# Optimization experiments

Hardware: AMD Instinct MI355X
Metric: run time of the kernel (lower is better)

Reference implementation:

```python
import jax, jax.numpy as jnp
import numpy as np

EMBED = 1024
HEADS = 16
HEAD_DIM = EMBED // HEADS
NEG = -1e20


def setup_inputs() -> dict:
    key = jax.random.key(0)
    ks = jax.random.split(key, 12)
    N, S, E = 2, 2048, EMBED
    w = lambda k: (jax.random.normal(k, (E, E), dtype=jnp.float32) * 0.02)
    b = lambda k: (jax.random.normal(k, (E,), dtype=jnp.float32) * 0.02)
    return {
        "values": jax.random.normal(ks[0], (N, S, E), dtype=jnp.float32),
        "keys": jax.random.normal(ks[1], (N, S, E), dtype=jnp.float32),
        "query": jax.random.normal(ks[2], (N, S, E), dtype=jnp.float32),
        "mask": jnp.ones((N, S), dtype=jnp.int32),
        "Wv": w(ks[3]), "bv": b(ks[4]),
        "Wk": w(ks[5]), "bk": b(ks[6]),
        "Wq": w(ks[7]), "bq": b(ks[8]),
        "Wo": w(ks[9]), "bo": b(ks[10]),
    }


def reference(values, keys, query, mask, Wv, bv, Wk, bk, Wq, bq, Wo, bo):
    N, S, E = query.shape
    # torch nn.Linear: x @ W.T + b
    v = (values @ Wv.T + bv).reshape(N, S, HEADS, HEAD_DIM)
    k = (keys @ Wk.T + bk).reshape(N, S, HEADS, HEAD_DIM)
    q = (query @ Wq.T + bq).reshape(N, S, HEADS, HEAD_DIM)
    # full [N,H,Q,K] score matrix, as in the original einsum
    energy = jnp.einsum('nqhd,nkhd->nhqk', q, k)
    # 2D mask with mismatched dims triggers causal tril path in the original
    causal = jnp.tril(jnp.ones((S, S), dtype=bool))  # [Q,K]
    energy = jnp.where(causal[None, None, :, :], energy, NEG)
    # NOTE: original scales by sqrt(embed_size), not sqrt(head_dim)
    attn = jax.nn.softmax(energy / jnp.sqrt(jnp.float32(E)), axis=3)
    out = jnp.einsum('nhqk,nkhd->nqhd', attn, v).reshape(N, S, E)
    return out @ Wo.T + bo
```

## Files before the change

kernel.cpp:

```cpp
#include <hip/hip_runtime.h>

typedef __bf16 bf16;
typedef __bf16 bf16x4 __attribute__((ext_vector_type(4)));
typedef __bf16 bf16x8 __attribute__((ext_vector_type(8)));
typedef float floatx4 __attribute__((ext_vector_type(4)));

#define GLOAD_LDS16(gp, lp) \
  __builtin_amdgcn_global_load_lds( \
      (const __attribute__((address_space(1))) void*)(gp), \
      (__attribute__((address_space(3))) void*)(lp), 16, 0, 0)

__global__ __launch_bounds__(256) void cvt_all_kernel(
    const float* __restrict__ v, const float* __restrict__ k, const float* __restrict__ q,
    const float* __restrict__ wv, const float* __restrict__ wk,
    const float* __restrict__ wq, const float* __restrict__ wo,
    bf16* __restrict__ xv, bf16* __restrict__ xk, bf16* __restrict__ xq,
    bf16* __restrict__ bwv, bf16* __restrict__ bwk, bf16* __restrict__ bwq,
    bf16* __restrict__ bwo) {
  const int i = blockIdx.x * 256 + threadIdx.x;
  const int A4 = 1 << 20;
  const float* src; bf16* dst; int off;
  if (i < A4)            { src = v; dst = xv; off = i; }
  else if (i < 2 * A4)   { src = k; dst = xk; off = i - A4; }
  else if (i < 3 * A4)   { src = q; dst = xq; off = i - 2 * A4; }
  else {
    int j = i - 3 * A4; int r = j >> 18; off = j & ((1 << 18) - 1);
    src = (r == 0) ? wv : (r == 1) ? wk : (r == 2) ? wq : wo;
    dst = (r == 0) ? bwv : (r == 1) ? bwk : (r == 2) ? bwq : bwo;
  }
  float4 x = reinterpret_cast<const float4*>(src)[off];
  union { bf16 b[4]; short4 s; } u;
  u.b[0] = (bf16)x.x; u.b[1] = (bf16)x.y; u.b[2] = (bf16)x.z; u.b[3] = (bf16)x.w;
  reinterpret_cast<short4*>(dst)[off] = u.s;
}

template <int MODE>
__device__ __forceinline__ void gemm_body(
    const bf16* __restrict__ A, const bf16* __restrict__ B,
    const float* __restrict__ bias, void* __restrict__ Cout,
    int bx, int by) {
  constexpr int K = 1024, N = 1024;
  __shared__ __align__(16) bf16 SMEM[8192];
  bf16* As = SMEM;
  bf16* Bs = SMEM + 4096;
  const int tid = threadIdx.x;
  const int lane = tid & 63;
  const int wave = tid >> 6;
  const int quad = lane >> 4;
  const int l16 = lane & 15;
  const int wm = (wave >> 1) * 64;
  const int wn = (wave & 1) * 64;
  const int am0 = by * 128;
  const int bn0 = bx * 128;
  const int srow = lane >> 2;
  const int scol = (lane & 3) * 8;

  floatx4 acc[4][4] = {};

  for (int k0 = 0; k0 < K; k0 += 32) {
    __syncthreads();
#pragma unroll
    for (int j = 0; j < 2; j++) {
      const int chunk = wave * 2 + j;
      const int row = chunk * 16 + srow;
      GLOAD_LDS16(A + (size_t)(am0 + row) * K + k0 + scol, As + chunk * 512);
      GLOAD_LDS16(B + (size_t)(bn0 + row) * K + k0 + scol, Bs + chunk * 512);
    }
    __syncthreads();

    bf16x8 af[4], bfv[4];
#pragma unroll
    for (int mi = 0; mi < 4; mi++)
      af[mi] = *reinterpret_cast<const bf16x8*>(&As[(wm + mi * 16 + l16) * 32 + quad * 8]);
#pragma unroll
    for (int ni = 0; ni < 4; ni++)
      bfv[ni] = *reinterpret_cast<const bf16x8*>(&Bs[(wn + ni * 16 + l16) * 32 + quad * 8]);
#pragma unroll
    for (int mi = 0; mi < 4; mi++)
#pragma unroll
      for (int ni = 0; ni < 4; ni++)
        acc[mi][ni] = __builtin_amdgcn_mfma_f32_16x16x32_bf16(af[mi], bfv[ni], acc[mi][ni], 0, 0, 0);
  }

  if constexpr (MODE == 2) {
#pragma unroll
    for (int mi = 0; mi < 4; mi++) {
#pragma unroll
      for (int ni = 0; ni < 4; ni++) {
        const int col = bn0 + wn + ni * 16 + l16;
        const float bb = bias[col];
        const int row = am0 + wm + mi * 16 + quad * 4;
#pragma unroll
        for (int r = 0; r < 4; r++)
          reinterpret_cast<float*>(Cout)[(size_t)(row + r) * N + col] = acc[mi][ni][r] + bb;
      }
    }
  } else {
    __syncthreads();
    bf16* T = SMEM + wave * 2048;
    const int nb = (am0 + wm) >> 11;
    const int sq0 = (am0 + wm) & 2047;
    const int h = (bn0 + wn) >> 6;
    const int nh = nb * 16 + h;
    const int r8 = lane >> 3, c8 = lane & 7;

    if constexpr (MODE == 0) {
#pragma unroll
      for (int pp = 0; pp < 2; pp++) {
#pragma unroll
        for (int mm = 0; mm < 2; mm++) {
          const int mi = pp * 2 + mm;
#pragma unroll
          for (int ni = 0; ni < 4; ni++) {
            const int d = ni * 16 + l16;
            const float bc = bias[bn0 + wn + d];
#pragma unroll
            for (int r = 0; r < 4; r++) {
              const int s = mm * 16 + quad * 4 + r;
              T[s * 64 + (d & 7) + 8 * ((d >> 3) ^ (s & 7))] = (bf16)(acc[mi][ni][r] + bc);
            }
          }
        }
#pragma unroll
        for (int it = 0; it < 4; it++) {
          const int s = it * 8 + r8;
          bf16x8 vv = *reinterpret_cast<const bf16x8*>(&T[s * 64 + ((c8 ^ r8) * 8)]);
          *reinterpret_cast<bf16x8*>(
              reinterpret_cast<bf16*>(Cout) +
              ((size_t)nh * 2048 + sq0 + pp * 32 + s) * 64 + c8 * 8) = vv;
        }
      }
    } else {
#pragma unroll
      for (int pp = 0; pp < 2; pp++) {
#pragma unroll
        for (int nn = 0; nn < 2; nn++) {
          const int ni = pp * 2 + nn;
          const int dp = nn * 16 + l16;
          const float bc = bias[bn0 + wn + pp * 32 + dp];
#pragma unroll
          for (int mi = 0; mi < 4; mi++) {
#pragma unroll
            for (int r = 0; r < 4; r++) {
              const int s = mi * 16 + quad * 4 + r;
              T[dp * 64 + (s & 7) + 8 * ((s >> 3) ^ (dp & 7))] = (bf16)(acc[mi][ni][r] + bc);
            }
          }
        }
#pragma unroll
        for (int it = 0; it < 4; it++) {
          const int dp = it * 8 + r8;
          bf16x8 vv = *reinterpret_cast<const bf16x8*>(&T[dp * 64 + ((c8 ^ r8) * 8)]);
          *reinterpret_cast<bf16x8*>(
              reinterpret_cast<bf16*>(Cout) +
              ((size_t)nh * 64 + pp * 32 + dp) * 2048 + sq0 + c8 * 8) = vv;
        }
      }
    }
  }
}

__global__ __launch_bounds__(256) void gemm_qkv(
    const bf16* __restrict__ A0, const bf16* __restrict__ B0, const float* __restrict__ c0, bf16* __restrict__ C0,
    const bf16* __restrict__ A1, const bf16* __restrict__ B1, const float* __restrict__ c1, bf16* __restrict__ C1,
    const bf16* __restrict__ A2, const bf16* __restrict__ B2, const float* __restrict__ c2, bf16* __restrict__ C2) {
  const int lin = blockIdx.x + (blockIdx.y << 3) + (blockIdx.z << 8);
  const int swz = (lin & 7) * 96 + (lin >> 3);
  const int bz = swz >> 8;
  const int by = (swz >> 3) & 31;
  const int bx = swz & 7;
  if (bz == 0)      gemm_body<0>(A0, B0, c0, C0, bx, by);
  else if (bz == 1) gemm_body<0>(A1, B1, c1, C1, bx, by);
  else              gemm_body<1>(A2, B2, c2, C2, bx, by);
}

__global__ __launch_bounds__(256) void gemm_out(
    const bf16* __restrict__ A, const bf16* __restrict__ B,
    const float* __restrict__ bias, float* __restrict__ C) {
  const int lin = blockIdx.x + (blockIdx.y << 3);
  const int swz = (lin & 7) * 32 + (lin >> 3);
  const int by = swz >> 3;
  const int bx = swz & 7;
  gemm_body<2>(A, B, bias, C, bx, by);
}

#define S_LEN 2048
#define EMB 1024
#define QT 128
#define KTILE 64
#define PSTR 72
#define SCALE2 (0.03125f * 1.44269504f)

__global__ __launch_bounds__(256) void attn_kernel(
    const bf16* __restrict__ Qh, const bf16* __restrict__ Kh,
    const bf16* __restrict__ Vt, bf16* __restrict__ O,
    float* __restrict__ Opart, float* __restrict__ lpart) {
  __shared__ __align__(16) bf16 Ks[2 * KTILE * 64];
  __shared__ __align__(16) bf16 Vs[2 * 64 * KTILE];
  __shared__ __align__(16) bf16 Ps[QT * PSTR];

  const int tid = threadIdx.x;
  const int lane = tid & 63;
  const int wave = tid >> 6;
  const int quad = lane >> 4;
  const int l16 = lane & 15;
  const int wq = wave * 32;

  const int c = blockIdx.x;
  const int role = blockIdx.y;
  const int nh = c >> 3;
  const int t = c & 7;
  const int n = nh >> 4;
  const int h = nh & 15;
  int qt, kt0, kt1;
  if (role == 0) { qt = t; kt0 = 0; kt1 = 2 * t + 2; }
  else {
    qt = 15 - t;
    const int halfk = qt + 1;
    kt0 = (role == 1) ? 0 : halfk;
    kt1 = (role == 1) ? halfk : 2 * halfk;
  }
  const int q0 = qt * QT;

  bf16x8 aq[2][2];
  {
    const bf16* Qb = Qh + ((size_t)nh * S_LEN + q0 + wq + l16) * 64 + quad * 8;
#pragma unroll
    for (int mi = 0; mi < 2; mi++)
#pragma unroll
      for (int kc = 0; kc < 2; kc++)
        aq[mi][kc] = *reinterpret_cast<const bf16x8*>(Qb + mi * 16 * 64 + kc * 32);
  }

  float l_part[2] = {};
  floatx4 o_acc[2][4] = {};

  const bf16* Kbase = Kh + (size_t)nh * S_LEN * 64;
  const bf16* Vbase = Vt + (size_t)nh * 64 * S_LEN;

  const int srl = lane >> 3;
  const int sc8 = lane & 7;

  auto stage = [&](int kt) {
    const int k0s = kt * KTILE;
    const int buf = (kt & 1) * 4096;
#pragma unroll
    for (int j = 0; j < 2; j++) {
      const int rl = wave * 16 + j * 8 + srl;
      const int c8s = ((sc8 ^ (rl & 7)) * 8);
      GLOAD_LDS16(Kbase + (size_t)(k0s + rl) * 64 + c8s, Ks + buf + (wave * 16 + j * 8) * 64);
      GLOAD_LDS16(Vbase + (size_t)rl * S_LEN + k0s + c8s, Vs + buf + (wave * 16 + j * 8) * 64);
    }
  };

  stage(kt0);
  for (int kt = kt0; kt < kt1; kt++) {
    const int k0 = kt * KTILE;
    __syncthreads();
    if (kt + 1 < kt1) stage(kt + 1);
    const bf16* Kc = Ks + (kt & 1) * 4096;
    const bf16* Vc = Vs + (kt & 1) * 4096;

    floatx4 s_acc[2][4] = {};
#pragma unroll
    for (int kc = 0; kc < 2; kc++) {
      bf16x8 bk[4];
#pragma unroll
      for (int ni = 0; ni < 4; ni++)
        bk[ni] = *reinterpret_cast<const bf16x8*>(
            &Kc[(ni * 16 + l16) * 64 + (((kc * 4 + quad) ^ (l16 & 7)) * 8)]);
#pragma unroll
      for (int mi = 0; mi < 2; mi++)
#pragma unroll
        for (int ni = 0; ni < 4; ni++)
          s_acc[mi][ni] = __builtin_amdgcn_mfma_f32_16x16x32_bf16(bk[ni], aq[mi][kc], s_acc[mi][ni], 0, 0, 0);
    }

    const bool needMask = (k0 + KTILE - 1) > (q0 + wq);
    const int qg = q0 + wq + l16;
#pragma unroll
    for (int mi = 0; mi < 2; mi++) {
#pragma unroll
      for (int ni = 0; ni < 4; ni++) {
        const int kgb = k0 + ni * 16 + quad * 4;
        bf16x4 pk;
#pragma unroll
        for (int r = 0; r < 4; r++) {
          float pr = __builtin_amdgcn_exp2f(s_acc[mi][ni][r] * SCALE2);
          if (needMask) pr = ((kgb + r) <= (qg + mi * 16)) ? pr : 0.f;
          l_part[mi] += pr;
          pk[r] = (bf16)pr;
        }
        *reinterpret_cast<bf16x4*>(
            &Ps[(wq + mi * 16 + l16) * PSTR + ni * 16 + quad * 4]) = pk;
      }
    }

#pragma unroll
    for (int kc = 0; kc < 2; kc++) {
      bf16x8 ap[2], bv[4];
#pragma unroll
      for (int mi = 0; mi < 2; mi++)
        ap[mi] = *reinterpret_cast<const bf16x8*>(
            &Ps[(wq + mi * 16 + l16) * PSTR + kc * 32 + quad * 8]);
#pragma unroll
      for (int di = 0; di < 4; di++)
        bv[di] = *reinterpret_cast<const bf16x8*>(
            &Vc[(di * 16 + l16) * 64 + (((kc * 4 + quad) ^ (l16 & 7)) * 8)]);
#pragma unroll
      for (int mi = 0; mi < 2; mi++)
#pragma unroll
        for (int di = 0; di < 4; di++)
          o_acc[mi][di] = __builtin_amdgcn_mfma_f32_16x16x32_bf16(ap[mi], bv[di], o_acc[mi][di], 0, 0, 0);
    }
  }

  float l_sum[2];
#pragma unroll
  for (int mi = 0; mi < 2; mi++) {
    float s = l_part[mi];
    s += __shfl_xor(s, 16);
    s += __shfl_xor(s, 32);
    l_sum[mi] = s;
  }

  if (role == 0) {
    bf16* Op = O + ((size_t)(n * S_LEN + q0 + wq)) * EMB + h * 64;
#pragma unroll
    for (int mi = 0; mi < 2; mi++) {
      const float linv = 1.0f / l_sum[mi];
#pragma unroll
      for (int r = 0; r < 4; r++) {
        const float inv = __shfl(linv, quad * 4 + r);
        bf16* orow = Op + (size_t)(mi * 16 + quad * 4 + r) * EMB;
#pragma unroll
        for (int di = 0; di < 4; di++)
          orow[di * 16 + l16] = (bf16)(o_acc[mi][di][r] * inv);
      }
    }
  } else {
    float* Ob = Opart + ((size_t)c * 2 + (role - 1)) * (QT * 64);
    float* lb = lpart + ((size_t)c * 2 + (role - 1)) * QT;
#pragma unroll
    for (int mi = 0; mi < 2; mi++)
      if (lane < 16) lb[wq + mi * 16 + lane] = l_sum[mi];
#pragma unroll
    for (int mi = 0; mi < 2; mi++)
#pragma unroll
      for (int r = 0; r < 4; r++) {
        float* orow = Ob + (size_t)(wq + mi * 16 + quad * 4 + r) * 64;
#pragma unroll
        for (int di = 0; di < 4; di++)
          orow[di * 16 + l16] = o_acc[mi][di][r];
      }
  }
}

__global__ __launch_bounds__(256) void attn_combine(
    const float* __restrict__ Opart, const float* __restrict__ lpart,
    bf16* __restrict__ O) {
  const int c = blockIdx.x;
  const int nh = c >> 3;
  const int t = c & 7;
  const int qt = 15 - t;
  const int n = nh >> 4;
  const int h = nh & 15;
  const float* O1 = Opart + (size_t)c * 2 * (QT * 64);
  const float* O2 = O1 + QT * 64;
  const float* l1 = lpart + (size_t)c * 2 * QT;
  const float* l2 = l1 + QT;
  const int tid = threadIdx.x;
  for (int i = tid; i < QT * 64 / 4; i += 256) {
    const int row = i >> 4;
    const float inv = 1.0f / (l1[row] + l2[row]);
    float4 a = reinterpret_cast<const float4*>(O1)[i];
    float4 b = reinterpret_cast<const float4*>(O2)[i];
    bf16x4 pk;
    pk[0] = (bf16)((a.x + b.x) * inv);
    pk[1] = (bf16)((a.y + b.y) * inv);
    pk[2] = (bf16)((a.z + b.z) * inv);
    pk[3] = (bf16)((a.w + b.w) * inv);
    *reinterpret_cast<bf16x4*>(
        O + ((size_t)(n * S_LEN + qt * QT + row)) * EMB + h * 64 + (i & 15) * 4) = pk;
  }
}

extern "C" void kernel_launch(void* const* d_in, const int* in_sizes, int n_in,
                              void* d_out, int out_size, void* d_ws, size_t ws_size,
                              hipStream_t stream) {
  (void)in_sizes; (void)n_in; (void)out_size; (void)ws_size;
  const float* values = (const float*)d_in[0];
  const float* keys   = (const float*)d_in[1];
  const float* query  = (const float*)d_in[2];
  const float* Wv = (const float*)d_in[4];
  const float* bv = (const float*)d_in[5];
  const float* Wk = (const float*)d_in[6];
  const float* bk = (const float*)d_in[7];
  const float* Wq = (const float*)d_in[8];
  const float* bq = (const float*)d_in[9];
  const float* Wo = (const float*)d_in[10];
  const float* bo = (const float*)d_in[11];
  float* out = (float*)d_out;

  const int NB = 2, S = 2048, E = 1024;
  const int M = NB * S;
  const size_t MB_ = 1u << 20;
  char* ws = (char*)d_ws;
  bf16* xv  = (bf16*)(ws + 0 * MB_);
  bf16* xk  = (bf16*)(ws + 8 * MB_);
  bf16* xq  = (bf16*)(ws + 16 * MB_);
  bf16* wvb = (bf16*)(ws + 24 * MB_);
  bf16* wkb = (bf16*)(ws + 26 * MB_);
  bf16* wqb = (bf16*)(ws + 28 * MB_);
  bf16* wob = (bf16*)(ws + 30 * MB_);
  bf16* kh  = (bf16*)(ws + 32 * MB_);
  bf16* qh  = (bf16*)(ws + 40 * MB_);
  bf16* vt  = (bf16*)(ws + 48 * MB_);
  bf16* ao  = (bf16*)(ws + 56 * MB_);
  float* Opart = (float*)(ws + 0 * MB_);
  float* lpart = (float*)(ws + 17 * MB_);

  cvt_all_kernel<<<(4 << 20) / 256, 256, 0, stream>>>(
      values, keys, query, Wv, Wk, Wq, Wo,
      xv, xk, xq, wvb, wkb, wqb, wob);

  gemm_qkv<<<dim3(E / 128, M / 128, 3), 256, 0, stream>>>(
      xq, wqb, bq, qh,
      xk, wkb, bk, kh,
      xv, wvb, bv, vt);

  attn_kernel<<<dim3(256, 3), 256, 0, stream>>>(qh, kh, vt, ao, Opart, lpart);
  attn_combine<<<dim3(256), 256, 0, stream>>>(Opart, lpart, ao);

  gemm_out<<<dim3(E / 128, M / 128), 256, 0, stream>>>(ao, wob, bo, out);
}
```

Before: 228.0 us.

## Double-buffer LDS tiles in the GEMM main loop via dynamic shared memory

The GEMM K-loop now uses two LDS buffers, so the async global-to-LDS load for the next K step is issued before the MFMA compute on the current buffer. This is meant to overlap memory latency with compute and halve the barrier count per K step. Shared memory moves to a dynamic 32 KB allocation, which lowers per-CU occupancy headroom. The epilogue's reuse of SMEM as scratch now indexes into the dynamic buffer.

```diff
diff --git a/kernel.cpp b/kernel.cpp
--- a/kernel.cpp
+++ b/kernel.cpp
@@ -38,11 +38,9 @@
 __device__ __forceinline__ void gemm_body(
     const bf16* __restrict__ A, const bf16* __restrict__ B,
     const float* __restrict__ bias, void* __restrict__ Cout,
-    int bx, int by) {
+    int bx, int by, bf16* __restrict__ SMEM) {
   constexpr int K = 1024, N = 1024;
-  __shared__ __align__(16) bf16 SMEM[8192];
-  bf16* As = SMEM;
-  bf16* Bs = SMEM + 4096;
+  constexpr int NSTEP = K / 32;
   const int tid = threadIdx.x;
   const int lane = tid & 63;
   const int wave = tid >> 6;
@@ -57,8 +55,10 @@
 
   floatx4 acc[4][4] = {};
 
-  for (int k0 = 0; k0 < K; k0 += 32) {
-    __syncthreads();
+  auto stage = [&](int step, int bufsel) {
+    const int k0 = step * 32;
+    bf16* As = SMEM + bufsel * 8192;
+    bf16* Bs = As + 4096;
 #pragma unroll
     for (int j = 0; j < 2; j++) {
       const int chunk = wave * 2 + j;
@@ -66,8 +66,11 @@
       GLOAD_LDS16(A + (size_t)(am0 + row) * K + k0 + scol, As + chunk * 512);
       GLOAD_LDS16(B + (size_t)(bn0 + row) * K + k0 + scol, Bs + chunk * 512);
     }
-    __syncthreads();
-
+  };
+
+  auto compute = [&](int bufsel) {
+    const bf16* As = SMEM + bufsel * 8192;
+    const bf16* Bs = As + 4096;
     bf16x8 af[4], bfv[4];
 #pragma unroll
     for (int mi = 0; mi < 4; mi++)
@@ -80,6 +83,16 @@
 #pragma unroll
       for (int ni = 0; ni < 4; ni++)
         acc[mi][ni] = __builtin_amdgcn_mfma_f32_16x16x32_bf16(af[mi], bfv[ni], acc[mi][ni], 0, 0, 0);
+  };
+
+  stage(0, 0);
+  for (int t = 0; t < NSTEP; t += 2) {
+    __syncthreads();
+    stage(t + 1, 1);
+    compute(0);
+    __syncthreads();
+    if (t + 2 < NSTEP) stage(t + 2, 0);
+    compute(1);
   }
 
   if constexpr (MODE == 2) {
@@ -164,24 +177,26 @@
     const bf16* __restrict__ A0, const bf16* __restrict__ B0, const float* __restrict__ c0, bf16* __restrict__ C0,
     const bf16* __restrict__ A1, const bf16* __restrict__ B1, const float* __restrict__ c1, bf16* __restrict__ C1,
     const bf16* __restrict__ A2, const bf16* __restrict__ B2, const float* __restrict__ c2, bf16* __restrict__ C2) {
+  extern __shared__ __align__(16) bf16 SMEM[];
   const int lin = blockIdx.x + (blockIdx.y << 3) + (blockIdx.z << 8);
   const int swz = (lin & 7) * 96 + (lin >> 3);
   const int bz = swz >> 8;
   const int by = (swz >> 3) & 31;
   const int bx = swz & 7;
-  if (bz == 0)      gemm_body<0>(A0, B0, c0, C0, bx, by);
-  else if (bz == 1) gemm_body<0>(A1, B1, c1, C1, bx, by);
-  else              gemm_body<1>(A2, B2, c2, C2, bx, by);
+  if (bz == 0)      gemm_body<0>(A0, B0, c0, C0, bx, by, SMEM);
+  else if (bz == 1) gemm_body<0>(A1, B1, c1, C1, bx, by, SMEM);
+  else              gemm_body<1>(A2, B2, c2, C2, bx, by, SMEM);
 }
 
 __global__ __launch_bounds__(256) void gemm_out(
     const bf16* __restrict__ A, const bf16* __restrict__ B,
     const float* __restrict__ bias, float* __restrict__ C) {
+  extern __shared__ __align__(16) bf16 SMEM[];
   const int lin = blockIdx.x + (blockIdx.y << 3);
   const int swz = (lin & 7) * 32 + (lin >> 3);
   const int by = swz >> 3;
   const int bx = swz & 7;
-  gemm_body<2>(A, B, bias, C, bx, by);
+  gemm_body<2>(A, B, bias, C, bx, by, SMEM);
 }
 
 #define S_LEN 2048
@@ -424,7 +439,7 @@
       values, keys, query, Wv, Wk, Wq, Wo,
       xv, xk, xq, wvb, wkb, wqb, wob);
 
-  gemm_qkv<<<dim3(E / 128, M / 128, 3), 256, 0, stream>>>(
+  gemm_qkv<<<dim3(E / 128, M / 128, 3), 256, 32768, stream>>>(
       xq, wqb, bq, qh,
       xk, wkb, bk, kh,
       xv, wvb, bv, vt);
@@ -432,5 +447,5 @@
   attn_kernel<<<dim3(256, 3), 256, 0, stream>>>(qh, kh, vt, ao, Opart, lpart);
   attn_combine<<<dim3(256), 256, 0, stream>>>(Opart, lpart, ao);
 
-  gemm_out<<<dim3(E / 128, M / 128), 256, 0, stream>>>(ao, wob, bo, out);
-}
+  gemm_out<<<dim3(E / 128, M / 128), 256, 32768, stream>>>(ao, wob, bo, out);
+}
```

Result: no change. 225.2 us (-1.2%).

## Fuse fp32-to-bf16 conversion into GEMM operand staging, drop convert kernel

Applied to the files above, without the earlier changes.

Removes the separate conversion kernel that wrote bf16 copies of the activations and weights. The QKV and output GEMMs now stage fp32 tiles straight into LDS with an XOR swizzle and convert to bf16 when building MFMA fragments. This saves a kernel launch and a full write-then-read round trip of the converted data. In exchange the GEMMs move twice the bytes per tile from global memory, use more LDS per block, and spend extra ALU on conversions inside the inner loop, every time each fp32 tile is reloaded.

```diff
diff --git a/kernel.cpp b/kernel.cpp
--- a/kernel.cpp
+++ b/kernel.cpp
@@ -10,39 +10,16 @@
       (const __attribute__((address_space(1))) void*)(gp), \
       (__attribute__((address_space(3))) void*)(lp), 16, 0, 0)
 
-__global__ __launch_bounds__(256) void cvt_all_kernel(
-    const float* __restrict__ v, const float* __restrict__ k, const float* __restrict__ q,
-    const float* __restrict__ wv, const float* __restrict__ wk,
-    const float* __restrict__ wq, const float* __restrict__ wo,
-    bf16* __restrict__ xv, bf16* __restrict__ xk, bf16* __restrict__ xq,
-    bf16* __restrict__ bwv, bf16* __restrict__ bwk, bf16* __restrict__ bwq,
-    bf16* __restrict__ bwo) {
-  const int i = blockIdx.x * 256 + threadIdx.x;
-  const int A4 = 1 << 20;
-  const float* src; bf16* dst; int off;
-  if (i < A4)            { src = v; dst = xv; off = i; }
-  else if (i < 2 * A4)   { src = k; dst = xk; off = i - A4; }
-  else if (i < 3 * A4)   { src = q; dst = xq; off = i - 2 * A4; }
-  else {
-    int j = i - 3 * A4; int r = j >> 18; off = j & ((1 << 18) - 1);
-    src = (r == 0) ? wv : (r == 1) ? wk : (r == 2) ? wq : wo;
-    dst = (r == 0) ? bwv : (r == 1) ? bwk : (r == 2) ? bwq : bwo;
-  }
-  float4 x = reinterpret_cast<const float4*>(src)[off];
-  union { bf16 b[4]; short4 s; } u;
-  u.b[0] = (bf16)x.x; u.b[1] = (bf16)x.y; u.b[2] = (bf16)x.z; u.b[3] = (bf16)x.w;
-  reinterpret_cast<short4*>(dst)[off] = u.s;
-}
-
-template <int MODE>
+template <int MODE, bool AF32>
 __device__ __forceinline__ void gemm_body(
-    const bf16* __restrict__ A, const bf16* __restrict__ B,
+    const void* __restrict__ Ain, const float* __restrict__ B,
     const float* __restrict__ bias, void* __restrict__ Cout,
-    int bx, int by) {
+    int bx, int by, bf16* __restrict__ SMEM) {
   constexpr int K = 1024, N = 1024;
-  __shared__ __align__(16) bf16 SMEM[8192];
-  bf16* As = SMEM;
-  bf16* Bs = SMEM + 4096;
+  float* Af = reinterpret_cast<float*>(SMEM);
+  bf16* Ab = SMEM;
+  float* Bf = reinterpret_cast<float*>(
+      reinterpret_cast<char*>(SMEM) + (AF32 ? 16384 : 8192));
   const int tid = threadIdx.x;
   const int lane = tid & 63;
   const int wave = tid >> 6;
@@ -52,29 +29,61 @@
   const int wn = (wave & 1) * 64;
   const int am0 = by * 128;
   const int bn0 = bx * 128;
-  const int srow = lane >> 2;
-  const int scol = (lane & 3) * 8;
+  const int srl8 = lane >> 3;
+  const int sc8 = lane & 7;
 
   floatx4 acc[4][4] = {};
+
+  auto stageF32 = [&](const float* G, int rowbase, float* Ls, int k0) {
+#pragma unroll
+    for (int j = 0; j < 4; j++) {
+      const int rg = wave * 32 + j * 8;
+      const int r = rg + srl8;
+      GLOAD_LDS16(G + (size_t)(rowbase + r) * K + k0 + ((sc8 ^ (r & 7)) << 2),
+                  Ls + rg * 32);
+    }
+  };
+  auto stageB16 = [&](const bf16* G, int rowbase, bf16* Ls, int k0) {
+#pragma unroll
+    for (int j = 0; j < 2; j++) {
+      const int chunk = wave * 2 + j;
+      const int row = chunk * 16 + (lane >> 2);
+      GLOAD_LDS16(G + (size_t)(rowbase + row) * K + k0 + (lane & 3) * 8,
+                  Ls + chunk * 512);
+    }
+  };
+  auto fragF32 = [&](const float* Ls, int r) -> bf16x8 {
+    const int q2 = quad * 2;
+    float4 lo = *reinterpret_cast<const float4*>(
+        &Ls[r * 32 + (((q2)     ^ (r & 7)) << 2)]);
+    float4 hi = *reinterpret_cast<const float4*>(
+        &Ls[r * 32 + (((q2 | 1) ^ (r & 7)) << 2)]);
+    bf16x8 v = {(bf16)lo.x, (bf16)lo.y, (bf16)lo.z, (bf16)lo.w,
+                (bf16)hi.x, (bf16)hi.y, (bf16)hi.z, (bf16)hi.w};
+    return v;
+  };
 
   for (int k0 = 0; k0 < K; k0 += 32) {
     __syncthreads();
-#pragma unroll
-    for (int j = 0; j < 2; j++) {
-      const int chunk = wave * 2 + j;
-      const int row = chunk * 16 + srow;
-      GLOAD_LDS16(A + (size_t)(am0 + row) * K + k0 + scol, As + chunk * 512);
-      GLOAD_LDS16(B + (size_t)(bn0 + row) * K + k0 + scol, Bs + chunk * 512);
-    }
+    if constexpr (AF32)
+      stageF32(reinterpret_cast<const float*>(Ain), am0, Af, k0);
+    else
+      stageB16(reinterpret_cast<const bf16*>(Ain), am0, Ab, k0);
+    stageF32(B, bn0, Bf, k0);
     __syncthreads();
 
     bf16x8 af[4], bfv[4];
 #pragma unroll
-    for (int mi = 0; mi < 4; mi++)
-      af[mi] = *reinterpret_cast<const bf16x8*>(&As[(wm + mi * 16 + l16) * 32 + quad * 8]);
+    for (int mi = 0; mi < 4; mi++) {
+      if constexpr (AF32)
+        af[mi] = fragF32(Af, wm + mi * 16 + l16);
+      else
+        af[mi] = *reinterpret_cast<const bf16x8*>(
+            &Ab[(wm + mi * 16 + l16) * 32 + quad * 8]);
+    }
 #pragma unroll
     for (int ni = 0; ni < 4; ni++)
-      bfv[ni] = *reinterpret_cast<const bf16x8*>(&Bs[(wn + ni * 16 + l16) * 32 + quad * 8]);
+      bfv[ni] = fragF32(Bf, wn + ni * 16 + l16);
 #pragma unroll
     for (int mi = 0; mi < 4; mi++)
 #pragma unroll
@@ -161,27 +170,29 @@
 }
 
 __global__ __launch_bounds__(256) void gemm_qkv(
-    const bf16* __restrict__ A0, const bf16* __restrict__ B0, const float* __restrict__ c0, bf16* __restrict__ C0,
-    const bf16* __restrict__ A1, const bf16* __restrict__ B1, const float* __restrict__ c1, bf16* __restrict__ C1,
-    const bf16* __restrict__ A2, const bf16* __restrict__ B2, const float* __restrict__ c2, bf16* __restrict__ C2) {
+    const float* __restrict__ A0, const float* __restrict__ B0, const float* __restrict__ c0, bf16* __restrict__ C0,
+    const float* __restrict__ A1, const float* __restrict__ B1, const float* __restrict__ c1, bf16* __restrict__ C1,
+    const float* __restrict__ A2, const float* __restrict__ B2, const float* __restrict__ c2, bf16* __restrict__ C2) {
+  extern __shared__ __align__(16) bf16 SMEM[];
   const int lin = blockIdx.x + (blockIdx.y << 3) + (blockIdx.z << 8);
   const int swz = (lin & 7) * 96 + (lin >> 3);
   const int bz = swz >> 8;
   const int by = (swz >> 3) & 31;
   const int bx = swz & 7;
-  if (bz == 0)      gemm_body<0>(A0, B0, c0, C0, bx, by);
-  else if (bz == 1) gemm_body<0>(A1, B1, c1, C1, bx, by);
-  else              gemm_body<1>(A2, B2, c2, C2, bx, by);
+  if (bz == 0)      gemm_body<0, true>(A0, B0, c0, C0, bx, by, SMEM);
+  else if (bz == 1) gemm_body<0, true>(A1, B1, c1, C1, bx, by, SMEM);
+  else              gemm_body<1, true>(A2, B2, c2, C2, bx, by, SMEM);
 }
 
 __global__ __launch_bounds__(256) void gemm_out(
-    const bf16* __restrict__ A, const bf16* __restrict__ B,
+    const bf16* __restrict__ A, const float* __restrict__ B,
     const float* __restrict__ bias, float* __restrict__ C) {
+  extern __shared__ __align__(16) bf16 SMEM[];
   const int lin = blockIdx.x + (blockIdx.y << 3);
   const int swz = (lin & 7) * 32 + (lin >> 3);
   const int by = swz >> 3;
   const int bx = swz & 7;
-  gemm_body<2>(A, B, bias, C, bx, by);
+  gemm_body<2, false>(A, B, bias, C, bx, by, SMEM);
 }
 
 #define S_LEN 2048
@@ -402,17 +413,10 @@
   const float* bo = (const float*)d_in[11];
   float* out = (float*)d_out;
 
-  const int NB = 2, S = 2048, E = 1024;
-  const int M = NB * S;
+  const int S = 2048, E = 1024;
+  const int M = 2 * S;
   const size_t MB_ = 1u << 20;
   char* ws = (char*)d_ws;
-  bf16* xv  = (bf16*)(ws + 0 * MB_);
-  bf16* xk  = (bf16*)(ws + 8 * MB_);
-  bf16* xq  = (bf16*)(ws + 16 * MB_);
-  bf16* wvb = (bf16*)(ws + 24 * MB_);
-  bf16* wkb = (bf16*)(ws + 26 * MB_);
-  bf16* wqb = (bf16*)(ws + 28 * MB_);
-  bf16* wob = (bf16*)(ws + 30 * MB_);
   bf16* kh  = (bf16*)(ws + 32 * MB_);
   bf16* qh  = (bf16*)(ws + 40 * MB_);
   bf16* vt  = (bf16*)(ws + 48 * MB_);
@@ -420,17 +424,13 @@
   float* Opart = (float*)(ws + 0 * MB_);
   float* lpart = (float*)(ws + 17 * MB_);
 
-  cvt_all_kernel<<<(4 << 20) / 256, 256, 0, stream>>>(
-      values, keys, query, Wv, Wk, Wq, Wo,
-      xv, xk, xq, wvb, wkb, wqb, wob);
-
-  gemm_qkv<<<dim3(E / 128, M / 128, 3), 256, 0, stream>>>(
-      xq, wqb, bq, qh,
-      xk, wkb, bk, kh,
-      xv, wvb, bv, vt);
+  gemm_qkv<<<dim3(E / 128, M / 128, 3), 256, 32768, stream>>>(
+      query, Wq, bq, qh,
+      keys, Wk, bk, kh,
+      values, Wv, bv, vt);
 
   attn_kernel<<<dim3(256, 3), 256, 0, stream>>>(qh, kh, vt, ao, Opart, lpart);
   attn_combine<<<dim3(256), 256, 0, stream>>>(Opart, lpart, ao);
 
-  gemm_out<<<dim3(E / 128, M / 128), 256, 0, stream>>>(ao, wob, bo, out);
-}
+  gemm_out<<<dim3(E / 128, M / 128), 256, 24576, stream>>>(ao, Wo, bo, out);
+}
```

New measurement: 276.0 us. +21.0%, slower.
